# Kernel optimization log

Measured on AMD Instinct MI355X. Metric: run time of the kernel, lower is better.

Reference implementation:

```python
import jax, jax.numpy as jnp
import numpy as np

WIN = 8   # window size
NH = 8    # n_heads


def _rel_pos_index(w):
    # Standard Swin relative position index table: [w*w, w*w] in [0, (2w-1)^2)
    coords = jnp.stack(jnp.meshgrid(jnp.arange(w), jnp.arange(w), indexing='ij'))  # [2,w,w]
    coords = coords.reshape(2, -1)  # [2, w*w]
    rel = coords[:, :, None] - coords[:, None, :]  # [2, w*w, w*w]
    rel = rel.transpose(1, 2, 0) + (w - 1)
    return rel[..., 0] * (2 * w - 1) + rel[..., 1]  # [w*w, w*w]


def setup_inputs() -> dict:
    key = jax.random.key(0)
    ks = jax.random.split(key, 6)
    C = 256
    return {
        'xs1': jax.random.normal(ks[0], (8, 64, 64, C), jnp.float32),
        'xs2': jax.random.normal(ks[1], (8, 32, 32, C), jnp.float32),
        'xq': jax.random.normal(ks[2], (8, 1024, C), jnp.float32),
        'W_qkv': jax.random.normal(ks[3], (C, 3 * C), jnp.float32) * 0.02,
        'b_qkv': jnp.zeros((3 * C,), jnp.float32),
        'W_proj': jax.random.normal(ks[4], (C, C), jnp.float32) * 0.02,
        'b_proj': jnp.zeros((C,), jnp.float32),
        'rel_pos_table': jax.random.normal(ks[5], ((2 * WIN - 1) ** 2, NH), jnp.float32) * 0.02,
    }


def reference(xs1, xs2, xq, W_qkv, b_qkv, W_proj, b_proj, rel_pos_table):
    B, H11, W11, C = xs1.shape
    _, H12, W12, _ = xs2.shape
    L11, L12, L2 = H11 * W11, H12 * W12, xq.shape[1]
    w, nh = WIN, NH
    hd = C // nh
    inv_sqrt_hd = 1.0 / jnp.sqrt(jnp.float32(hd))

    # joint QKV projection over concatenated tokens
    xsq = jnp.concatenate([xs1.reshape(B, L11, C), xs2.reshape(B, L12, C), xq], axis=1)
    qkv = xsq @ W_qkv + b_qkv  # [B, L11+L12+L2, 3C]

    # ---- windowed self-attention on xs1 ----
    xs_qkv = qkv[:, :L11].reshape(B, H11 // w, w, W11 // w, w, 3 * C)
    xs_qkv = xs_qkv.transpose(0, 1, 3, 2, 4, 5).reshape(-1, w * w, 3, nh, hd)  # [Bw, w^2, 3, nh, hd]
    xs_qkv = xs_qkv.transpose(2, 0, 3, 1, 4)  # [3, Bw, nh, w^2, hd]
    q, k, v = xs_qkv[0] * inv_sqrt_hd, xs_qkv[1], xs_qkv[2]
    scores = jnp.einsum('bhqd,bhkd->bhqk', q, k)  # [Bw, nh, w^2, w^2]
    bias = rel_pos_table[_rel_pos_index(w)]  # [w^2, w^2, nh]
    scores = scores + bias.transpose(2, 0, 1)[None]
    # original code divides by sqrt(head_features) again after the q scale
    probs = jax.nn.softmax(scores * inv_sqrt_hd, axis=-1)
    xs_out = jnp.einsum('bhqk,bhkd->bhqd', probs, v)  # [Bw, nh, w^2, hd]
    xs_out = xs_out.transpose(0, 2, 1, 3).reshape(-1, w, w, C)
    # window reverse
    xs_out = xs_out.reshape(B, H11 // w, W11 // w, w, w, C)
    xs_out = xs_out.transpose(0, 1, 3, 2, 4, 5).reshape(B, L11, C)

    # ---- cross attention: xq queries attend to [xs2 kv ; xq kv] ----
    xq_qkv = qkv[:, L11 + L12:].reshape(B, L2, 3, nh, hd).transpose(2, 0, 3, 1, 4)  # [3,B,nh,L2,hd]
    xq_q, xq_k, xq_v = xq_qkv[0], xq_qkv[1], xq_qkv[2]
    xs2_qkv = qkv[:, L11:L11 + L12].reshape(B, L12, 3, nh, hd).transpose(2, 0, 3, 1, 4)
    k2 = jnp.concatenate([xs2_qkv[1], xq_k], axis=2)  # [B,nh,L12+L2,hd]
    v2 = jnp.concatenate([xs2_qkv[2], xq_v], axis=2)
    # NOTE: original does NOT apply q_scale here, only the /sqrt(hd) divide
    cscores = jnp.einsum('bhqd,bhkd->bhqk', xq_q, k2) * inv_sqrt_hd
    cprobs = jax.nn.softmax(cscores, axis=-1)
    xq_out = jnp.einsum('bhqk,bhkd->bhqd', cprobs, v2)  # [B,nh,L2,hd]
    xq_out = xq_out.transpose(0, 2, 1, 3).reshape(B, L2, C)

    out = jnp.concatenate([xs_out, xq_out], axis=1) @ W_proj + b_proj  # [B, L11+L2, C]
    return out
```

## Files before the change

### kernel.cpp

```cpp
#include <hip/hip_runtime.h>
#include <hip/hip_bf16.h>

typedef unsigned short u16;
typedef unsigned int u32;
typedef __attribute__((ext_vector_type(8))) __bf16 bf16x8;
typedef __attribute__((ext_vector_type(4))) float f32x4;

#define INV_HD  0.03125f
#define INV_SHD 0.17677669529663687f
#define LOG2E   1.4426950408889634f

__device__ __forceinline__ float b2f(u16 u) {
  union { u32 i; float f; } v; v.i = ((u32)u) << 16; return v.f;
}
__device__ __forceinline__ u16 f2b(float f) {
  union { float f; u32 i; } v; v.f = f;
  u32 x = v.i;
  return (u16)((x + 0x7fffu + ((x >> 16) & 1u)) >> 16);
}
__device__ __forceinline__ bf16x8 ld16(const u16* p) {
  return *reinterpret_cast<const bf16x8*>(p);
}
union U8 { bf16x8 v; u16 s[8]; };
__device__ __forceinline__ u32 cvtpk(float a, float b) {
  u32 r;
  asm("v_cvt_pk_bf16_f32 %0, %1, %2" : "=v"(r) : "v"(a), "v"(b));
  return r;
}
__device__ __forceinline__ float pl32add(float x) {
  union { float f; u32 u; } c; c.f = x;
  auto r = __builtin_amdgcn_permlane32_swap(c.u, c.u, false, false);
  union { u32 u; float f; } a, b; a.u = r[0]; b.u = r[1];
  return a.f + b.f;
}
__device__ __forceinline__ float pl16add(float x) {
#if __has_builtin(__builtin_amdgcn_permlane16_swap)
  union { float f; u32 u; } c; c.f = x;
  auto r = __builtin_amdgcn_permlane16_swap(c.u, c.u, false, false);
  union { u32 u; float f; } a, b; a.u = r[0]; b.u = r[1];
  return a.f + b.f;
#else
  return x + __shfl_xor(x, 16, 64);
#endif
}

__global__ __launch_bounds__(256) void kPrep(
    const float* __restrict__ xs1, const float* __restrict__ xs2, const float* __restrict__ xq,
    const float* __restrict__ Wqkv, const float* __restrict__ Wproj, const float* __restrict__ tblg,
    u16* __restrict__ Abf, u16* __restrict__ WTq, u16* __restrict__ WTp, u16* __restrict__ BiasC)
{
  const int bx = blockIdx.x, tid = threadIdx.x;
  if (bx < 6144) {
    int t = bx * 256 + tid;
    int row = t >> 5, c8 = (t & 31) * 8;
    int b = row / 6144, r = row - b * 6144;
    const float* src;
    if (r < 4096)      src = xs1 + ((size_t)b * 4096 + r) * 256;
    else if (r < 5120) src = xs2 + ((size_t)b * 1024 + (r - 4096)) * 256;
    else               src = xq  + ((size_t)b * 1024 + (r - 5120)) * 256;
    U8 u;
#pragma unroll
    for (int j = 0; j < 8; ++j) u.s[j] = f2b(src[c8 + j]);
    *reinterpret_cast<bf16x8*>(Abf + (size_t)row * 256 + c8) = u.v;
  } else if (bx < 6912) {
    int i = (bx - 6144) * 256 + tid;
    int n = i >> 8, k = i & 255;
    WTq[i] = f2b(Wqkv[(size_t)k * 768 + n]);
  } else if (bx < 7168) {
    int i = (bx - 6912) * 256 + tid;
    int n = i >> 8, k = i & 255;
    WTp[i] = f2b(Wproj[(size_t)k * 256 + n]);
  } else {
    int gid = (bx - 7168) * 256 + tid;
    int lane = gid & 63, t = gid >> 6;
    int h = t >> 4, qt = (t >> 2) & 3, kt = t & 3;
    int lr = lane & 15, kg = lane >> 4;
    int q = qt * 16 + lr;
    int qi = q >> 3, qj = q & 7;
    ushort4 out;
#pragma unroll
    for (int i = 0; i < 4; ++i) {
      int key = kt * 16 + kg * 4 + i;
      int ki = key >> 3, kj = key & 7;
      int idx = (qi - ki + 7) * 15 + (qj - kj + 7);
      ((u16*)&out)[i] = f2b(tblg[idx * 8 + h] * (INV_SHD * LOG2E));
    }
    *reinterpret_cast<ushort4*>(BiasC + (size_t)(t * 64 + lane) * 4) = out;
  }
}

__global__ __launch_bounds__(256, 2) void kQKV(
    const u16* __restrict__ Abf,
    const u16* __restrict__ WT, const float* __restrict__ bias,
    u16* __restrict__ qk, u16* __restrict__ VT, u16* __restrict__ VST)
{
  __shared__ u16 St[4][9216];
  const int tid = threadIdx.x;
  const int lane = tid & 63, wid = tid >> 6;
  const int lr = lane & 15, kg = lane >> 4;
  const int m0 = blockIdx.x * 256 + wid * 64;
  const int by = blockIdx.y;
  const int m0blk = blockIdx.x * 256;
  const int bb = m0blk / 6144, rloc = m0blk - bb * 6144;
  u16* S = St[wid];

  bf16x8 a[4][8];
#pragma unroll
  for (int mt = 0; mt < 4; ++mt) {
    const u16* asrc = Abf + (size_t)(m0 + mt * 16 + lr) * 256 + kg * 8;
#pragma unroll
    for (int ks = 0; ks < 8; ++ks) a[mt][ks] = ld16(asrc + ks * 32);
  }

  const int n0 = (by < 4) ? by * 128 : 512 + (by - 4) * 128;
  const u16* bcol0 = WT + (size_t)(n0 + lr) * 256 + kg * 8;

  bf16x8 bq[2][8];
#pragma unroll
  for (int ks = 0; ks < 8; ++ks) bq[0][ks] = ld16(bcol0 + ks * 32);

  if (by < 4) {
    const float qsc = (by < 2) ? (INV_SHD * LOG2E) : 1.f;
#pragma unroll
    for (int nt = 0; nt < 8; ++nt) {
      const int cur = nt & 1, nxt = cur ^ 1;
      if (nt + 1 < 8) {
        const u16* bp = bcol0 + (size_t)(nt + 1) * 16 * 256;
#pragma unroll
        for (int ks = 0; ks < 8; ++ks) bq[nxt][ks] = ld16(bp + ks * 32);
      }
      f32x4 acc[4] = {{0.f,0.f,0.f,0.f},{0.f,0.f,0.f,0.f},{0.f,0.f,0.f,0.f},{0.f,0.f,0.f,0.f}};
#pragma unroll
      for (int ks = 0; ks < 8; ++ks) {
#pragma unroll
        for (int mt = 0; mt < 4; ++mt)
          acc[mt] = __builtin_amdgcn_mfma_f32_16x16x32_bf16(a[mt][ks], bq[cur][ks], acc[mt], 0, 0, 0);
      }
      float bv = bias[n0 + nt * 16 + lr];
#pragma unroll
      for (int mt = 0; mt < 4; ++mt)
#pragma unroll
        for (int i = 0; i < 4; ++i)
          S[(mt * 16 + kg * 4 + i) * 136 + nt * 16 + lr] = f2b((acc[mt][i] + bv) * qsc);
    }
#pragma unroll
    for (int p = 0; p < 16; ++p) {
      bf16x8 v = *reinterpret_cast<const bf16x8*>(&S[(p * 4 + kg) * 136 + lr * 8]);
      *reinterpret_cast<bf16x8*>(qk + (size_t)(m0 + p * 4 + kg) * 512 + n0 + lr * 8) = v;
    }
  } else {
    const bool isWin = (rloc < 4096);
    u16* Vb = isWin ? (VST + (size_t)bb * 256 * 4096) : (VT + (size_t)bb * 256 * 2048);
    const int VS = isWin ? 4096 : 2048;
    const int tokwave = (isWin ? rloc : (rloc - 4096)) + wid * 64;
#pragma unroll
    for (int nt = 0; nt < 8; ++nt) {
      const int cur = nt & 1, nxt = cur ^ 1;
      if (nt + 1 < 8) {
        const u16* bp = bcol0 + (size_t)(nt + 1) * 16 * 256;
#pragma unroll
        for (int ks = 0; ks < 8; ++ks) bq[nxt][ks] = ld16(bp + ks * 32);
      }
      f32x4 acc[4] = {{0.f,0.f,0.f,0.f},{0.f,0.f,0.f,0.f},{0.f,0.f,0.f,0.f},{0.f,0.f,0.f,0.f}};
#pragma unroll
      for (int ks = 0; ks < 8; ++ks) {
#pragma unroll
        for (int mt = 0; mt < 4; ++mt)
          acc[mt] = __builtin_amdgcn_mfma_f32_16x16x32_bf16(bq[cur][ks], a[mt][ks], acc[mt], 0, 0, 0);
      }
      float4 bv4 = *reinterpret_cast<const float4*>(bias + n0 + nt * 16 + kg * 4);
      const float* bvp = (const float*)&bv4;
#pragma unroll
      for (int mt = 0; mt < 4; ++mt)
#pragma unroll
        for (int i = 0; i < 4; ++i) {
          int c = nt * 16 + kg * 4 + i;
          S[c * 72 + mt * 16 + lr] = f2b(acc[mt][i] + bvp[i]);
        }
    }
#pragma unroll
    for (int p = 0; p < 8; ++p) {
#pragma unroll
      for (int half = 0; half < 2; ++half) {
        bf16x8 v = *reinterpret_cast<const bf16x8*>(&S[(p * 16 + lr) * 72 + half * 32 + kg * 8]);
        *reinterpret_cast<bf16x8*>(
            Vb + (size_t)((by - 4) * 128 + p * 16 + lr) * VS + tokwave + half * 32 + kg * 8) = v;
      }
    }
  }
}

__device__ __forceinline__ void selfQT(
    int qt, bf16x8 qfq, const bf16x8 (&kf)[4],
    const u16* __restrict__ BiasC, int h, int lane, int lr, int kg, u16* P)
{
  f32x4 st[4];
#pragma unroll
  for (int kt = 0; kt < 4; ++kt) {
    f32x4 z = {0.f,0.f,0.f,0.f};
    st[kt] = __builtin_amdgcn_mfma_f32_16x16x32_bf16(kf[kt], qfq, z, 0, 0, 0);
  }
  const float c0 = INV_SHD;
  float lsum = 0.f;
#pragma unroll
  for (int kt = 0; kt < 4; ++kt) {
    ushort4 bv = *reinterpret_cast<const ushort4*>(
        BiasC + (size_t)((h * 16 + qt * 4 + kt) * 64 + lane) * 4);
    st[kt][0] = exp2f(st[kt][0] * c0 + b2f(bv.x));
    st[kt][1] = exp2f(st[kt][1] * c0 + b2f(bv.y));
    st[kt][2] = exp2f(st[kt][2] * c0 + b2f(bv.z));
    st[kt][3] = exp2f(st[kt][3] * c0 + b2f(bv.w));
    lsum += st[kt][0] + st[kt][1] + st[kt][2] + st[kt][3];
  }
  lsum = pl16add(lsum);
  lsum = pl32add(lsum);
  float inv = 1.f / lsum;
#pragma unroll
  for (int kt = 0; kt < 4; ++kt) {
    u32 w0 = cvtpk(st[kt][0] * inv, st[kt][1] * inv);
    u32 w1 = cvtpk(st[kt][2] * inv, st[kt][3] * inv);
    *reinterpret_cast<uint2*>(&P[lr * 72 + kt * 16 + kg * 4]) = make_uint2(w0, w1);
  }
}

__device__ __forceinline__ void cload(
    const u16* __restrict__ kbase, const u16* __restrict__ vbase, int kc0, int lr, int kg,
    bf16x8 (&kf)[4], bf16x8 (&vf)[4])
{
#pragma unroll
  for (int kt = 0; kt < 4; ++kt)
    kf[kt] = ld16(kbase + (size_t)(kc0 + kt * 16 + lr) * 512);
#pragma unroll
  for (int ks = 0; ks < 2; ++ks) {
    vf[ks]     = ld16(vbase + (size_t)lr * 2048 + kc0 + ks * 32 + kg * 8);
    vf[2 + ks] = ld16(vbase + (size_t)(16 + lr) * 2048 + kc0 + ks * 32 + kg * 8);
  }
}

__device__ __forceinline__ void cstep(
    const bf16x8 (&kf)[4], const bf16x8 (&vf)[4], bf16x8 qf,
    u16* P, int lr, int kg, f32x4& o0, f32x4& o1, float& l)
{
  f32x4 st[4];
#pragma unroll
  for (int kt = 0; kt < 4; ++kt) {
    f32x4 z = {0.f,0.f,0.f,0.f};
    st[kt] = __builtin_amdgcn_mfma_f32_16x16x32_bf16(kf[kt], qf, z, 0, 0, 0);
  }
  float lsum = 0.f;
#pragma unroll
  for (int kt = 0; kt < 4; ++kt) {
    st[kt][0] = exp2f(st[kt][0]);
    st[kt][1] = exp2f(st[kt][1]);
    st[kt][2] = exp2f(st[kt][2]);
    st[kt][3] = exp2f(st[kt][3]);
    lsum += st[kt][0] + st[kt][1] + st[kt][2] + st[kt][3];
  }
  lsum = pl16add(lsum);
  l += pl32add(lsum);
#pragma unroll
  for (int kt = 0; kt < 4; ++kt) {
    u32 w0 = cvtpk(st[kt][0], st[kt][1]);
    u32 w1 = cvtpk(st[kt][2], st[kt][3]);
    *reinterpret_cast<uint2*>(&P[lr * 72 + kt * 16 + kg * 4]) = make_uint2(w0, w1);
  }
#pragma unroll
  for (int ks = 0; ks < 2; ++ks) {
    bf16x8 pf = ld16(P + lr * 72 + ks * 32 + kg * 8);
    o0 = __builtin_amdgcn_mfma_f32_16x16x32_bf16(pf, vf[ks],     o0, 0, 0, 0);
    o1 = __builtin_amdgcn_mfma_f32_16x16x32_bf16(pf, vf[2 + ks], o1, 0, 0, 0);
  }
}

__global__ __launch_bounds__(256) void kAttn(
    const u16* __restrict__ qk, const u16* __restrict__ BiasC,
    const u16* __restrict__ VST, const u16* __restrict__ VT,
    u16* __restrict__ X, u16* __restrict__ Opart, float* __restrict__ L)
{
  __shared__ u16 Pl[4][2304];
  const int tid = threadIdx.x;
  const int lane = tid & 63, wid = tid >> 6;
  const int lr = lane & 15, kg = lane >> 4;
  const int bx = blockIdx.x;

  if (bx < 2048) {
    const int bh = bx & 63, b = bh >> 3, h = bh & 7;
    const int qy = (bx >> 6) & 7, s = bx >> 9;
    const int q0 = qy * 128 + wid * 16;
    const size_t qrow0 = (size_t)b * 6144 + 5120;
    const size_t krow0 = (size_t)b * 6144 + 4096;
    const size_t srow = (s < 2) ? (krow0 + s * 512) : (qrow0 + (s - 2) * 512);
    const u16* kbase = qk + srow * 512 + 256 + h * 32 + kg * 8;
    const u16* vbase = VT + (size_t)bh * 32 * 2048 + s * 512;
    u16* PA = Pl[wid];
    u16* PB = Pl[wid] + 1152;

    bf16x8 qfA = ld16(qk + (qrow0 + q0      + lr) * 512 + h * 32 + kg * 8);
    bf16x8 qfB = ld16(qk + (qrow0 + q0 + 64 + lr) * 512 + h * 32 + kg * 8);

    f32x4 oA0 = {0.f,0.f,0.f,0.f}, oA1 = {0.f,0.f,0.f,0.f};
    f32x4 oB0 = {0.f,0.f,0.f,0.f}, oB1 = {0.f,0.f,0.f,0.f};
    float lA = 0.f, lB = 0.f;

#pragma unroll 1
    for (int ck = 0; ck < 8; ++ck) {
      bf16x8 kf[4], vf[4];
      cload(kbase, vbase, ck * 64, lr, kg, kf, vf);
      cstep(kf, vf, qfA, PA, lr, kg, oA0, oA1, lA);
      cstep(kf, vf, qfB, PB, lr, kg, oB0, oB1, lB);
    }

    const size_t rowb = (size_t)(s * 64 + bh) * 1024;
#pragma unroll
    for (int i = 0; i < 4; ++i) {
      int qa = q0 + kg * 4 + i, qb = qa + 64;
      Opart[(rowb + qa) * 32 + lr]      = f2b(oA0[i]);
      Opart[(rowb + qa) * 32 + 16 + lr] = f2b(oA1[i]);
      Opart[(rowb + qb) * 32 + lr]      = f2b(oB0[i]);
      Opart[(rowb + qb) * 32 + 16 + lr] = f2b(oB1[i]);
    }
    if (kg == 0) {
      L[rowb + q0 + lr]      = lA;
      L[rowb + q0 + 64 + lr] = lB;
    }
  } else {
    const int bid = bx - 2048;
    const int w = bid >> 1;
    const int h = (bid & 1) * 4 + wid;
    const int b = w >> 6, wz = w & 63;
    const int wy = wz >> 3, wx = wz & 7;
    const size_t tokbase = (size_t)b * 6144 + wy * 512 + wx * 8;
    const size_t xbase   = (size_t)b * 5120 + wy * 512 + wx * 8;
    u16* P = Pl[wid];

    bf16x8 qf[4], kf[4];
#pragma unroll
    for (int t4 = 0; t4 < 4; ++t4) {
      int t = t4 * 16 + lr;
      size_t row = tokbase + (t >> 3) * 64 + (t & 7);
      const u16* p = qk + row * 512 + h * 32 + kg * 8;
      qf[t4] = ld16(p);
      kf[t4] = ld16(p + 256);
    }
    bf16x8 vf[2][2];
#pragma unroll
    for (int dt = 0; dt < 2; ++dt)
#pragma unroll
      for (int ks = 0; ks < 2; ++ks)
        vf[dt][ks] = ld16(VST + ((size_t)(b * 8 + h) * 32 + dt * 16 + lr) * 4096
                          + (wy * 8 + ks * 4 + kg) * 64 + wx * 8);

    f32x4 o[4][2] = {};
#pragma unroll
    for (int qt = 0; qt < 4; ++qt) {
      selfQT(qt, qf[qt], kf, BiasC, h, lane, lr, kg, P);
#pragma unroll
      for (int ks = 0; ks < 2; ++ks) {
        bf16x8 pf = ld16(P + lr * 72 + ks * 32 + kg * 8);
        o[qt][0] = __builtin_amdgcn_mfma_f32_16x16x32_bf16(pf, vf[0][ks], o[qt][0], 0, 0, 0);
        o[qt][1] = __builtin_amdgcn_mfma_f32_16x16x32_bf16(pf, vf[1][ks], o[qt][1], 0, 0, 0);
      }
    }
#pragma unroll
    for (int qt = 0; qt < 4; ++qt)
#pragma unroll
      for (int i = 0; i < 4; ++i) {
        int t = qt * 16 + kg * 4 + i;
        size_t xrow = xbase + (t >> 3) * 64 + (t & 7);
#pragma unroll
        for (int dt = 0; dt < 2; ++dt)
          X[xrow * 256 + h * 32 + dt * 16 + lr] = f2b(o[qt][dt][i]);
      }
  }
}

__global__ __launch_bounds__(256) void kComb(
    const u16* __restrict__ Opart, const float* __restrict__ L, u16* __restrict__ X)
{
  int gid = blockIdx.x * 256 + threadIdx.x;
  int row = gid >> 2;
  int dp = (gid & 3) * 8;
  int bh = row >> 10, q = row & 1023;
  int b = bh >> 3, h = bh & 7;
  float lsum = L[row] + L[65536 + row] + L[131072 + row] + L[196608 + row];
  float inv = 1.f / lsum;
  float acc[8] = {0.f,0.f,0.f,0.f,0.f,0.f,0.f,0.f};
#pragma unroll
  for (int s = 0; s < 4; ++s) {
    U8 a;
    a.v = ld16(Opart + ((size_t)(s * 65536 + row) * 32 + dp));
#pragma unroll
    for (int j = 0; j < 8; ++j) acc[j] += b2f(a.s[j]);
  }
  U8 r;
#pragma unroll
  for (int j = 0; j < 8; ++j) r.s[j] = f2b(acc[j] * inv);
  size_t xrow = (size_t)b * 5120 + 4096 + q;
  *reinterpret_cast<bf16x8*>(X + xrow * 256 + h * 32 + dp) = r.v;
}

__global__ __launch_bounds__(256) void kProj(
    const u16* __restrict__ Xin, const u16* __restrict__ WT, const float* __restrict__ bias,
    float* __restrict__ out)
{
  const int tid = threadIdx.x;
  const int lane = tid & 63, wid = tid >> 6;
  const int lr = lane & 15, kg = lane >> 4;
  const int m0 = blockIdx.x * 128 + wid * 32;
  const int n0 = blockIdx.y * 128;
  bf16x8 a[2][8];
#pragma unroll
  for (int mt = 0; mt < 2; ++mt) {
    const u16* src = Xin + (size_t)(m0 + mt * 16 + lr) * 256 + kg * 8;
#pragma unroll
    for (int ks = 0; ks < 8; ++ks) a[mt][ks] = ld16(src + ks * 32);
  }
  for (int nt = 0; nt < 8; ++nt) {
    const int n = n0 + nt * 16;
    const u16* bp = WT + (size_t)(n + lr) * 256 + kg * 8;
    f32x4 acc0 = {0.f,0.f,0.f,0.f}, acc1 = {0.f,0.f,0.f,0.f};
#pragma unroll
    for (int ks = 0; ks < 8; ++ks) {
      bf16x8 bq = ld16(bp + ks * 32);
      acc0 = __builtin_amdgcn_mfma_f32_16x16x32_bf16(a[0][ks], bq, acc0, 0, 0, 0);
      acc1 = __builtin_amdgcn_mfma_f32_16x16x32_bf16(a[1][ks], bq, acc1, 0, 0, 0);
    }
    float bv = bias[n + lr];
#pragma unroll
    for (int i = 0; i < 4; ++i) {
      int r0 = m0 + kg * 4 + i;
      out[(size_t)r0 * 256 + n + lr]        = acc0[i] + bv;
      out[(size_t)(r0 + 16) * 256 + n + lr] = acc1[i] + bv;
    }
  }
}

extern "C" void kernel_launch(void* const* d_in, const int* in_sizes, int n_in,
                              void* d_out, int out_size, void* d_ws, size_t ws_size,
                              hipStream_t stream)
{
  const float* xs1   = (const float*)d_in[0];
  const float* xs2   = (const float*)d_in[1];
  const float* xq    = (const float*)d_in[2];
  const float* Wqkv  = (const float*)d_in[3];
  const float* bqkv  = (const float*)d_in[4];
  const float* Wproj = (const float*)d_in[5];
  const float* bproj = (const float*)d_in[6];
  const float* tbl   = (const float*)d_in[7];

  u16* ws  = (u16*)d_ws;
  u16* qk  = ws;
  u16* X   = qk + 25165824;
  u16* WTq = X + 10485760;
  u16* WTp = WTq + 196608;
  u16* VT  = WTp + 65536;
  u16* VST = VT + 4194304;

  u16*   BiasC = (u16*)d_out;
  float* L     = (float*)((char*)d_out + 262144);
  u16*   Abf   = (u16*)((char*)d_out + 1310720);
  u16*   Opart = (u16*)((char*)d_out + 1310720);

  kPrep<<<7200, 256, 0, stream>>>(xs1, xs2, xq, Wqkv, Wproj, tbl, Abf, WTq, WTp, BiasC);
  kQKV<<<dim3(192, 6), 256, 0, stream>>>(Abf, WTq, bqkv, qk, VT, VST);
  kAttn<<<3072, 256, 0, stream>>>(qk, BiasC, VST, VT, X, Opart, L);
  kComb<<<1024, 256, 0, stream>>>(Opart, L, X);
  kProj<<<dim3(320, 2), 256, 0, stream>>>(X, WTp, bproj, (float*)d_out);
}
```

Measured before the change: 195.7 us.

## Enlarge per-wave tiles in cross-attention and projection, halve KV splits

The cross-attention blocks now handle 64 queries per wave instead of 32 and split the key range into 2 chunks instead of 4. Each K/V chunk load is therefore reused across four query tiles, and the combine kernel reduces only two partials. The projection kernel uses 64-row tiles per wave and double-buffers its weight fragments in registers to cut redundant weight loads and hide latency. The cost is more registers and fewer blocks (launch bounds set to 3), which lowers parallelism and may reduce occupancy.

```diff
diff --git a/kernel.cpp b/kernel.cpp
--- a/kernel.cpp
+++ b/kernel.cpp
@@ -272,59 +272,62 @@
   }
 }
 
-__global__ __launch_bounds__(256) void kAttn(
+__global__ __launch_bounds__(256, 3) void kAttn(
     const u16* __restrict__ qk, const u16* __restrict__ BiasC,
     const u16* __restrict__ VST, const u16* __restrict__ VT,
     u16* __restrict__ X, u16* __restrict__ Opart, float* __restrict__ L)
 {
-  __shared__ u16 Pl[4][2304];
+  __shared__ u16 Pl[4][4608];
   const int tid = threadIdx.x;
   const int lane = tid & 63, wid = tid >> 6;
   const int lr = lane & 15, kg = lane >> 4;
   const int bx = blockIdx.x;
 
-  if (bx < 2048) {
+  if (bx < 512) {
     const int bh = bx & 63, b = bh >> 3, h = bh & 7;
-    const int qy = (bx >> 6) & 7, s = bx >> 9;
-    const int q0 = qy * 128 + wid * 16;
+    const int qy = (bx >> 6) & 3, s = bx >> 8;
+    const int qw = qy * 256 + wid * 64;
     const size_t qrow0 = (size_t)b * 6144 + 5120;
     const size_t krow0 = (size_t)b * 6144 + 4096;
-    const size_t srow = (s < 2) ? (krow0 + s * 512) : (qrow0 + (s - 2) * 512);
-    const u16* kbase = qk + srow * 512 + 256 + h * 32 + kg * 8;
-    const u16* vbase = VT + (size_t)bh * 32 * 2048 + s * 512;
-    u16* PA = Pl[wid];
-    u16* PB = Pl[wid] + 1152;
-
-    bf16x8 qfA = ld16(qk + (qrow0 + q0      + lr) * 512 + h * 32 + kg * 8);
-    bf16x8 qfB = ld16(qk + (qrow0 + q0 + 64 + lr) * 512 + h * 32 + kg * 8);
-
-    f32x4 oA0 = {0.f,0.f,0.f,0.f}, oA1 = {0.f,0.f,0.f,0.f};
-    f32x4 oB0 = {0.f,0.f,0.f,0.f}, oB1 = {0.f,0.f,0.f,0.f};
-    float lA = 0.f, lB = 0.f;
+    const u16* kbase = qk + ((s ? qrow0 : krow0) * 512) + 256 + h * 32 + kg * 8;
+    const u16* vbase = VT + (size_t)bh * 32 * 2048 + s * 1024;
+    u16* P = Pl[wid];
+
+    bf16x8 qf[4];
+#pragma unroll
+    for (int t = 0; t < 4; ++t)
+      qf[t] = ld16(qk + (qrow0 + qw + t * 16 + lr) * 512 + h * 32 + kg * 8);
+
+    f32x4 o[4][2] = {};
+    float l[4] = {0.f, 0.f, 0.f, 0.f};
 
 #pragma unroll 1
-    for (int ck = 0; ck < 8; ++ck) {
+    for (int ck = 0; ck < 16; ++ck) {
       bf16x8 kf[4], vf[4];
       cload(kbase, vbase, ck * 64, lr, kg, kf, vf);
-      cstep(kf, vf, qfA, PA, lr, kg, oA0, oA1, lA);
-      cstep(kf, vf, qfB, PB, lr, kg, oB0, oB1, lB);
+      cstep(kf, vf, qf[0], P,        lr, kg, o[0][0], o[0][1], l[0]);
+      cstep(kf, vf, qf[1], P + 1152, lr, kg, o[1][0], o[1][1], l[1]);
+      cstep(kf, vf, qf[2], P + 2304, lr, kg, o[2][0], o[2][1], l[2]);
+      cstep(kf, vf, qf[3], P + 3456, lr, kg, o[3][0], o[3][1], l[3]);
     }
 
     const size_t rowb = (size_t)(s * 64 + bh) * 1024;
 #pragma unroll
-    for (int i = 0; i < 4; ++i) {
-      int qa = q0 + kg * 4 + i, qb = qa + 64;
-      Opart[(rowb + qa) * 32 + lr]      = f2b(oA0[i]);
-      Opart[(rowb + qa) * 32 + 16 + lr] = f2b(oA1[i]);
-      Opart[(rowb + qb) * 32 + lr]      = f2b(oB0[i]);
-      Opart[(rowb + qb) * 32 + 16 + lr] = f2b(oB1[i]);
+    for (int t = 0; t < 4; ++t) {
+#pragma unroll
+      for (int i = 0; i < 4; ++i) {
+        int qa = qw + t * 16 + kg * 4 + i;
+        Opart[(rowb + qa) * 32 + lr]      = f2b(o[t][0][i]);
+        Opart[(rowb + qa) * 32 + 16 + lr] = f2b(o[t][1][i]);
+      }
     }
     if (kg == 0) {
-      L[rowb + q0 + lr]      = lA;
-      L[rowb + q0 + 64 + lr] = lB;
+#pragma unroll
+      for (int t = 0; t < 4; ++t)
+        L[rowb + qw + t * 16 + lr] = l[t];
     }
   } else {
-    const int bid = bx - 2048;
+    const int bid = bx - 512;
     const int w = bid >> 1;
     const int h = (bid & 1) * 4 + wid;
     const int b = w >> 6, wz = w & 63;
@@ -382,11 +385,11 @@
   int dp = (gid & 3) * 8;
   int bh = row >> 10, q = row & 1023;
   int b = bh >> 3, h = bh & 7;
-  float lsum = L[row] + L[65536 + row] + L[131072 + row] + L[196608 + row];
+  float lsum = L[row] + L[65536 + row];
   float inv = 1.f / lsum;
   float acc[8] = {0.f,0.f,0.f,0.f,0.f,0.f,0.f,0.f};
 #pragma unroll
-  for (int s = 0; s < 4; ++s) {
+  for (int s = 0; s < 2; ++s) {
     U8 a;
     a.v = ld16(Opart + ((size_t)(s * 65536 + row) * 32 + dp));
 #pragma unroll
@@ -399,39 +402,50 @@
   *reinterpret_cast<bf16x8*>(X + xrow * 256 + h * 32 + dp) = r.v;
 }
 
-__global__ __launch_bounds__(256) void kProj(
+__global__ __launch_bounds__(256, 3) void kProj(
     const u16* __restrict__ Xin, const u16* __restrict__ WT, const float* __restrict__ bias,
     float* __restrict__ out)
 {
   const int tid = threadIdx.x;
   const int lane = tid & 63, wid = tid >> 6;
   const int lr = lane & 15, kg = lane >> 4;
-  const int m0 = blockIdx.x * 128 + wid * 32;
+  const int m0 = blockIdx.x * 256 + wid * 64;
   const int n0 = blockIdx.y * 128;
-  bf16x8 a[2][8];
-#pragma unroll
-  for (int mt = 0; mt < 2; ++mt) {
+  bf16x8 a[4][8];
+#pragma unroll
+  for (int mt = 0; mt < 4; ++mt) {
     const u16* src = Xin + (size_t)(m0 + mt * 16 + lr) * 256 + kg * 8;
 #pragma unroll
     for (int ks = 0; ks < 8; ++ks) a[mt][ks] = ld16(src + ks * 32);
   }
+  const u16* bcol0 = WT + (size_t)(n0 + lr) * 256 + kg * 8;
+  bf16x8 bq[2][8];
+#pragma unroll
+  for (int ks = 0; ks < 8; ++ks) bq[0][ks] = ld16(bcol0 + ks * 32);
+#pragma unroll
   for (int nt = 0; nt < 8; ++nt) {
+    const int cur = nt & 1, nxt = cur ^ 1;
+    if (nt + 1 < 8) {
+      const u16* bp = bcol0 + (size_t)(nt + 1) * 16 * 256;
+#pragma unroll
+      for (int ks = 0; ks < 8; ++ks) bq[nxt][ks] = ld16(bp + ks * 32);
+    }
+    f32x4 acc[4] = {{0.f,0.f,0.f,0.f},{0.f,0.f,0.f,0.f},{0.f,0.f,0.f,0.f},{0.f,0.f,0.f,0.f}};
+#pragma unroll
+    for (int ks = 0; ks < 8; ++ks) {
+#pragma unroll
+      for (int mt = 0; mt < 4; ++mt)
+        acc[mt] = __builtin_amdgcn_mfma_f32_16x16x32_bf16(a[mt][ks], bq[cur][ks], acc[mt], 0, 0, 0);
+    }
     const int n = n0 + nt * 16;
-    const u16* bp = WT + (size_t)(n + lr) * 256 + kg * 8;
-    f32x4 acc0 = {0.f,0.f,0.f,0.f}, acc1 = {0.f,0.f,0.f,0.f};
-#pragma unroll
-    for (int ks = 0; ks < 8; ++ks) {
-      bf16x8 bq = ld16(bp + ks * 32);
-      acc0 = __builtin_amdgcn_mfma_f32_16x16x32_bf16(a[0][ks], bq, acc0, 0, 0, 0);
-      acc1 = __builtin_amdgcn_mfma_f32_16x16x32_bf16(a[1][ks], bq, acc1, 0, 0, 0);
-    }
     float bv = bias[n + lr];
 #pragma unroll
-    for (int i = 0; i < 4; ++i) {
-      int r0 = m0 + kg * 4 + i;
-      out[(size_t)r0 * 256 + n + lr]        = acc0[i] + bv;
-      out[(size_t)(r0 + 16) * 256 + n + lr] = acc1[i] + bv;
-    }
+    for (int mt = 0; mt < 4; ++mt)
+#pragma unroll
+      for (int i = 0; i < 4; ++i) {
+        int r0 = m0 + mt * 16 + kg * 4 + i;
+        out[(size_t)r0 * 256 + n + lr] = acc[mt][i] + bv;
+      }
   }
 }
 
@@ -463,7 +477,7 @@
 
   kPrep<<<7200, 256, 0, stream>>>(xs1, xs2, xq, Wqkv, Wproj, tbl, Abf, WTq, WTp, BiasC);
   kQKV<<<dim3(192, 6), 256, 0, stream>>>(Abf, WTq, bqkv, qk, VT, VST);
-  kAttn<<<3072, 256, 0, stream>>>(qk, BiasC, VST, VT, X, Opart, L);
+  kAttn<<<1536, 256, 0, stream>>>(qk, BiasC, VST, VT, X, Opart, L);
   kComb<<<1024, 256, 0, stream>>>(Opart, L, X);
-  kProj<<<dim3(320, 2), 256, 0, stream>>>(X, WTp, bproj, (float*)d_out);
-}
+  kProj<<<dim3(160, 2), 256, 0, stream>>>(X, WTp, bproj, (float*)d_out);
+}
```

Result: faster. 191.6 us (-2.1%).
